# Performance work log

Hardware: AMD Instinct MI355X
Metric: run time of the kernel (lower is better)

Reference implementation:

```python
import jax, jax.numpy as jnp
import numpy as np

N_NODES = 100000
N_EDGES = 1000000
IN_FEATS = 256
OUT_FEATS = 64


def setup_inputs() -> dict:
    key = jax.random.key(0)
    k1, k2, k3, k4 = jax.random.split(key, 4)
    x = jax.random.normal(k1, (N_NODES, IN_FEATS), dtype=jnp.float32)
    src = jax.random.randint(k2, (N_EDGES,), 0, N_NODES, dtype=jnp.int64)
    dst = jax.random.randint(k3, (N_EDGES,), 0, N_NODES, dtype=jnp.int64)
    # Glorot-style init as in dgl GraphConv
    W = jax.random.normal(k4, (IN_FEATS, OUT_FEATS), dtype=jnp.float32) * (2.0 / (IN_FEATS + OUT_FEATS)) ** 0.5
    b = jnp.zeros((OUT_FEATS,), dtype=jnp.float32)
    return {"x": x, "src": src, "dst": dst, "W": W, "b": b}


def reference(x, src, dst, W, b):
    # dgl GraphConv with norm='both':
    #   h = D_in^{-1/2} * A * D_out^{-1/2} * X * W + b
    # in_feats > out_feats -> dense transform first, then sparse aggregation.
    n = x.shape[0]
    e_ones = jnp.ones(src.shape[0], dtype=x.dtype)
    deg_out = jnp.clip(jax.ops.segment_sum(e_ones, src, num_segments=n), 1.0)  # [N]
    deg_in = jnp.clip(jax.ops.segment_sum(e_ones, dst, num_segments=n), 1.0)   # [N]
    h = (x * deg_out[:, None] ** -0.5) @ W                 # [N, out]
    agg = jax.ops.segment_sum(h[src], dst, num_segments=n)  # SpMM: [N, out]
    return agg * deg_in[:, None] ** -0.5 + b
```

## Files before the change

kernel.cpp:

```cpp
#include <hip/hip_runtime.h>

#define IN_F 256
#define OUT_F 64
#define BLK1 1024
#define BKT 128
#define CAP 4096

typedef __attribute__((ext_vector_type(8))) short s16x8;
typedef __attribute__((ext_vector_type(4))) float f32x4;
typedef __attribute__((ext_vector_type(4))) unsigned u32x4;

__device__ __forceinline__ unsigned short bf16_rne(float f) {
    unsigned u = __builtin_bit_cast(unsigned, f);
    u += 0x7FFFu + ((u >> 16) & 1u);
    return (unsigned short)(u >> 16);
}
__device__ __forceinline__ float bf16_lo(unsigned u) {
    return __builtin_bit_cast(float, u << 16);
}
__device__ __forceinline__ float bf16_hi(unsigned u) {
    return __builtin_bit_cast(float, u & 0xFFFF0000u);
}
__device__ __forceinline__ unsigned pk2(float a, float b) {
    unsigned r;
    asm("v_cvt_pk_bf16_f32 %0, %1, %2" : "=v"(r) : "v"(a), "v"(b));
    return r;
}

__global__ __launch_bounds__(512) void k_coarse(const int* __restrict__ src,
                                                const int* __restrict__ dst,
                                                int* __restrict__ cnt,
                                                int nb, int ne) {
    __shared__ int hD[1024], hS[1024];
    const int blk = blockIdx.x, tid = threadIdx.x;
    for (int i = tid; i < 1024; i += 512) { hD[i] = 0; hS[i] = 0; }
    __syncthreads();
    const int epb = (ne + BLK1 - 1) / BLK1;
    const int e0 = blk * epb, e1 = min(ne, e0 + epb);
    for (int e = e0 + tid; e < e1; e += 512) {
        atomicAdd(&hD[dst[e] >> 7], 1);
        atomicAdd(&hS[src[e] >> 7], 1);
    }
    __syncthreads();
    for (int bb = tid; bb < nb; bb += 512) {
        cnt[bb * BLK1 + blk] = hD[bb];
        cnt[(nb + bb) * BLK1 + blk] = hS[bb];
    }
}

__global__ __launch_bounds__(256) void k_scan1(const int* __restrict__ deg,
                                               int* __restrict__ excl,
                                               int* __restrict__ partials) {
    __shared__ int sd[256];
    const int tid = threadIdx.x;
    const int idx = blockIdx.x * 2048 + tid * 8;
    int4 va = *(const int4*)&deg[idx];
    int4 vb = *(const int4*)&deg[idx + 4];
    const int tsum = va.x + va.y + va.z + va.w + vb.x + vb.y + vb.z + vb.w;
    sd[tid] = tsum;
    __syncthreads();
    for (int off = 1; off < 256; off <<= 1) {
        int t = (tid >= off) ? sd[tid - off] : 0;
        __syncthreads();
        sd[tid] += t;
        __syncthreads();
    }
    int run = sd[tid] - tsum;
    if (tid == 255) partials[blockIdx.x] = sd[255];
    int4 oa, ob;
    oa.x = run; run += va.x;
    oa.y = run; run += va.y;
    oa.z = run; run += va.z;
    oa.w = run; run += va.w;
    ob.x = run; run += vb.x;
    ob.y = run; run += vb.y;
    ob.z = run; run += vb.z;
    ob.w = run;
    *(int4*)&excl[idx] = oa;
    *(int4*)&excl[idx + 4] = ob;
}

__global__ __launch_bounds__(1024) void k_scan2(int* __restrict__ partials, int nb) {
    __shared__ int sd[1024];
    const int tid = threadIdx.x;
    const int v = (tid < nb) ? partials[tid] : 0;
    sd[tid] = v;
    __syncthreads();
    for (int off = 1; off < 1024; off <<= 1) {
        int t = (tid >= off) ? sd[tid - off] : 0;
        __syncthreads();
        sd[tid] += t;
        __syncthreads();
    }
    if (tid < nb) partials[tid] = sd[tid] - v;
}

__global__ __launch_bounds__(512) void k_part(const int* __restrict__ src,
                                              const int* __restrict__ dst,
                                              const int* __restrict__ cnt,
                                              const int* __restrict__ partials,
                                              unsigned* __restrict__ tmpD,
                                              unsigned char* __restrict__ tmpS,
                                              int nb, int ne) {
    __shared__ int cD[1024], cS[1024];
    const int blk = blockIdx.x, tid = threadIdx.x;
    for (int bb = tid; bb < nb; bb += 512) {
        int iD = bb * BLK1 + blk;
        int iS = (nb + bb) * BLK1 + blk;
        cD[bb] = cnt[iD] + partials[iD >> 11];
        cS[bb] = cnt[iS] + partials[iS >> 11];
    }
    __syncthreads();
    const int epb = (ne + BLK1 - 1) / BLK1;
    const int e0 = blk * epb, e1 = min(ne, e0 + epb);
    for (int e = e0 + tid; e < e1; e += 512) {
        int d = dst[e], s = src[e];
        int pD = atomicAdd(&cD[d >> 7], 1);
        tmpD[pD] = ((unsigned)(d & 127) << 17) | (unsigned)s;
        int pS = atomicAdd(&cS[s >> 7], 1);
        tmpS[pS - ne] = (unsigned char)(s & 127);
    }
}

__global__ __launch_bounds__(256) void k_fine_src(const int* __restrict__ cnt,
                                                  const int* __restrict__ partials,
                                                  const unsigned char* __restrict__ tmpS,
                                                  int* __restrict__ deg_out,
                                                  int n, int nb, int ne) {
    __shared__ int hist[BKT];
    const int b = blockIdx.x, tid = threadIdx.x;
    const int ib = (nb + b) * BLK1;
    const int base = cnt[ib] + partials[ib >> 11] - ne;
    const int ie = (nb + b + 1) * BLK1;
    const int end = (b + 1 < nb) ? (cnt[ie] + partials[ie >> 11] - ne) : ne;
    if (tid < BKT) hist[tid] = 0;
    __syncthreads();
    for (int i = base + tid; i < end; i += 256)
        atomicAdd(&hist[tmpS[i] & 127u], 1);
    __syncthreads();
    const int node = b * BKT + tid;
    if (tid < BKT && node < n) deg_out[node] = hist[tid];
}

__global__ __launch_bounds__(256, 4) void k_gemm(const float* __restrict__ x,
                                                 const float* __restrict__ W,
                                                 const int* __restrict__ deg_out,
                                                 unsigned short* __restrict__ h, int n) {
    __shared__ char lds[32768];
    const int tid = threadIdx.x;
    const int lane = tid & 63;
    const int wid = tid >> 6;

    {
        const int f = tid & 63;
        const int kg = (tid >> 6) * 64;
        const int swz = (f & 7) << 4;
#pragma unroll
        for (int j = 0; j < 16; ++j) {
            const int k0 = kg + j * 4;
            float w0 = W[(k0 + 0) * OUT_F + f];
            float w1 = W[(k0 + 1) * OUT_F + f];
            float w2 = W[(k0 + 2) * OUT_F + f];
            float w3 = W[(k0 + 3) * OUT_F + f];
            uint2 p;
            p.x = pk2(w0, w1);
            p.y = pk2(w2, w3);
            *(uint2*)(lds + f * 512 + ((k0 * 2) ^ swz)) = p;
        }
    }
    __syncthreads();

    const int r15 = lane & 15;
    const int q = lane >> 4;
    const int bswz = (r15 & 7) << 4;
    const int b_base = r15 * 512;
    const int rq = q * 4;

#pragma unroll
    for (int p = 0; p < 2; ++p) {
        const int row = blockIdx.x * 128 + p * 64 + wid * 16 + r15;
        const int rowc = min(row, n - 1);
        const float* xr = x + (size_t)rowc * IN_F + q * 8;

        f32x4 acc0 = {0.f, 0.f, 0.f, 0.f};
        f32x4 acc1 = acc0, acc2 = acc0, acc3 = acc0;

#pragma unroll
        for (int kk = 0; kk < 8; ++kk) {
            float4 a0 = *(const float4*)(xr + kk * 32);
            float4 a1 = *(const float4*)(xr + kk * 32 + 4);
            u32x4 au;
            au[0] = pk2(a0.x, a0.y);
            au[1] = pk2(a0.z, a0.w);
            au[2] = pk2(a1.x, a1.y);
            au[3] = pk2(a1.z, a1.w);
            s16x8 a = __builtin_bit_cast(s16x8, au);
            const int off = (q * 16 + kk * 64) ^ bswz;
            s16x8 b0 = *(const s16x8*)(lds + b_base + off);
            s16x8 b1 = *(const s16x8*)(lds + b_base + 8192 + off);
            s16x8 b2 = *(const s16x8*)(lds + b_base + 16384 + off);
            s16x8 b3 = *(const s16x8*)(lds + b_base + 24576 + off);
            acc0 = __builtin_amdgcn_mfma_f32_16x16x32_bf16(a, b0, acc0, 0, 0, 0);
            acc1 = __builtin_amdgcn_mfma_f32_16x16x32_bf16(a, b1, acc1, 0, 0, 0);
            acc2 = __builtin_amdgcn_mfma_f32_16x16x32_bf16(a, b2, acc2, 0, 0, 0);
            acc3 = __builtin_amdgcn_mfma_f32_16x16x32_bf16(a, b3, acc3, 0, 0, 0);
        }

#pragma unroll
        for (int j = 0; j < 4; ++j) {
            const int grow = blockIdx.x * 128 + p * 64 + wid * 16 + rq + j;
            if (grow < n) {
                const float s = rsqrtf(fmaxf((float)deg_out[grow], 1.0f));
                unsigned short* hp = h + (size_t)grow * OUT_F + r15;
                hp[0]  = bf16_rne(acc0[j] * s);
                hp[16] = bf16_rne(acc1[j] * s);
                hp[32] = bf16_rne(acc2[j] * s);
                hp[48] = bf16_rne(acc3[j] * s);
            }
        }
    }
}

__global__ __launch_bounds__(512) void k_agg(const int* __restrict__ cnt,
                                             const int* __restrict__ partials,
                                             const unsigned* __restrict__ tmpD,
                                             const unsigned* __restrict__ h32,
                                             const float* __restrict__ b,
                                             float* __restrict__ out,
                                             int n, int nb, int ne) {
    __shared__ int hist[BKT], sd[BKT], cur[BKT], stt[BKT];
    __shared__ unsigned raw[CAP];
    __shared__ int eidx[CAP];
    const int bkt = blockIdx.x, tid = threadIdx.x;
    const int ib = bkt * BLK1;
    const int base = cnt[ib] + partials[ib >> 11];
    const int ie = (bkt + 1) * BLK1;
    const int end = (bkt + 1 < nb) ? (cnt[ie] + partials[ie >> 11]) : ne;
    const int cnt_e = min(end - base, CAP);

    if (tid < BKT) hist[tid] = 0;
    __syncthreads();
    for (int i = tid; i < cnt_e; i += 512) {
        unsigned v = tmpD[base + i];
        raw[i] = v;
        atomicAdd(&hist[v >> 17], 1);
    }
    __syncthreads();
    int dg0 = 0;
    if (tid < BKT) { dg0 = hist[tid]; sd[tid] = dg0; }
    __syncthreads();
    for (int off = 1; off < BKT; off <<= 1) {
        int t = 0;
        if (tid < BKT && tid >= off) t = sd[tid - off];
        __syncthreads();
        if (tid < BKT) sd[tid] += t;
        __syncthreads();
    }
    if (tid < BKT) {
        const int excl = sd[tid] - dg0;
        cur[tid] = excl;
        stt[tid] = excl;
    }
    __syncthreads();
    for (int i = tid; i < cnt_e; i += 512) {
        unsigned v = raw[i];
        int pos = atomicAdd(&cur[v >> 17], 1);
        eidx[min(pos, CAP - 1)] = (int)(v & 0x1FFFFu);
    }
    __syncthreads();

    const int wid = tid >> 6, lane = tid & 63;
    const int f2 = lane & 31, half = lane >> 5;
    for (int nd = wid; nd < BKT; nd += 8) {
        const int node = bkt * BKT + nd;
        if (node >= n) continue;
        const int st = stt[nd];
        const int dg = hist[nd];
        float a0 = 0.f, a1 = 0.f, c0 = 0.f, c1 = 0.f;
        float d0 = 0.f, d1 = 0.f, e0 = 0.f, e1 = 0.f;
        int i = 0;
        const int dg8 = dg & ~7;
        for (; i < dg8; i += 8) {
            int s0 = eidx[st + i + half];
            int s1 = eidx[st + i + 2 + half];
            int s2 = eidx[st + i + 4 + half];
            int s3 = eidx[st + i + 6 + half];
            unsigned u0 = h32[s0 * 32 + f2];
            unsigned u1 = h32[s1 * 32 + f2];
            unsigned u2 = h32[s2 * 32 + f2];
            unsigned u3 = h32[s3 * 32 + f2];
            a0 += bf16_lo(u0); a1 += bf16_hi(u0);
            c0 += bf16_lo(u1); c1 += bf16_hi(u1);
            d0 += bf16_lo(u2); d1 += bf16_hi(u2);
            e0 += bf16_lo(u3); e1 += bf16_hi(u3);
        }
        for (; i < dg; i += 2) {
            const int e = i + half;
            const bool v = e < dg;
            int s = eidx[st + (v ? e : i)];
            unsigned u = h32[s * 32 + f2];
            if (v) { a0 += bf16_lo(u); a1 += bf16_hi(u); }
        }
        a0 += c0; a1 += c1;
        d0 += e0; d1 += e1;
        a0 += d0; a1 += d1;
        a0 += __shfl_xor(a0, 32, 64);
        a1 += __shfl_xor(a1, 32, 64);
        if (half == 0) {
            const float scale = rsqrtf(fmaxf((float)dg, 1.0f));
            float2 v;
            v.x = a0 * scale + b[f2 * 2];
            v.y = a1 * scale + b[f2 * 2 + 1];
            *(float2*)&out[(size_t)node * OUT_F + f2 * 2] = v;
        }
    }
}

extern "C" void kernel_launch(void* const* d_in, const int* in_sizes, int n_in,
                              void* d_out, int out_size, void* d_ws, size_t ws_size,
                              hipStream_t stream) {
    const float* x   = (const float*)d_in[0];
    const int*   src = (const int*)d_in[1];
    const int*   dst = (const int*)d_in[2];
    const float* W   = (const float*)d_in[3];
    const float* b   = (const float*)d_in[4];
    float* out = (float*)d_out;

    const int n  = in_sizes[0] / IN_F;
    const int ne = in_sizes[1];

    const int nb = (n + BKT - 1) / BKT;
    const int m  = 2 * nb * BLK1;

    int* cnt          = (int*)d_ws;
    int* partials     = cnt + m;
    unsigned* tmpD    = (unsigned*)(partials + 1024);
    unsigned char* tmpS = (unsigned char*)(tmpD + ne);
    int* deg_out      = (int*)(tmpS + ((ne + 15) & ~15));
    unsigned short* h = (unsigned short*)(deg_out + n);

    const int nb_scan = m / 2048;

    k_coarse<<<BLK1, 512, 0, stream>>>(src, dst, cnt, nb, ne);
    k_scan1<<<nb_scan, 256, 0, stream>>>(cnt, cnt, partials);
    k_scan2<<<1, 1024, 0, stream>>>(partials, nb_scan);
    k_part<<<BLK1, 512, 0, stream>>>(src, dst, cnt, partials, tmpD, tmpS, nb, ne);
    k_fine_src<<<nb, 256, 0, stream>>>(cnt, partials, tmpS, deg_out, n, nb, ne);
    k_gemm<<<(n + 127) / 128, 256, 0, stream>>>(x, W, deg_out, h, n);
    k_agg<<<nb, 512, 0, stream>>>(cnt, partials, tmpD, (const unsigned*)h, b, out, n, nb, ne);
}
```

Measured before the change: 117.4 us.

## Fuse out-degree histogram into GEMM kernel and halve partition block count

Removes the separate k_fine_src kernel: each GEMM block now builds the out-degree histogram for its 128-node bucket in shared memory and applies the rsqrt scaling from LDS, dropping a launch and the deg_out global round trip. The partitioning pipeline also moves from 1024 blocks of 512 threads to 512 blocks of 256 threads. That shrinks the count matrix and the scan, with the scan indexing adjusted to match. The price is that the histogram pass now sits at the start of the GEMM, and the partition kernels have less parallelism.

```diff
diff --git a/kernel.cpp b/kernel.cpp
--- a/kernel.cpp
+++ b/kernel.cpp
@@ -2,7 +2,7 @@
 
 #define IN_F 256
 #define OUT_F 64
-#define BLK1 1024
+#define BLK1 512
 #define BKT 128
 #define CAP 4096
 
@@ -27,22 +27,22 @@
     return r;
 }
 
-__global__ __launch_bounds__(512) void k_coarse(const int* __restrict__ src,
+__global__ __launch_bounds__(256) void k_coarse(const int* __restrict__ src,
                                                 const int* __restrict__ dst,
                                                 int* __restrict__ cnt,
                                                 int nb, int ne) {
     __shared__ int hD[1024], hS[1024];
     const int blk = blockIdx.x, tid = threadIdx.x;
-    for (int i = tid; i < 1024; i += 512) { hD[i] = 0; hS[i] = 0; }
+    for (int i = tid; i < 1024; i += 256) { hD[i] = 0; hS[i] = 0; }
     __syncthreads();
     const int epb = (ne + BLK1 - 1) / BLK1;
     const int e0 = blk * epb, e1 = min(ne, e0 + epb);
-    for (int e = e0 + tid; e < e1; e += 512) {
+    for (int e = e0 + tid; e < e1; e += 256) {
         atomicAdd(&hD[dst[e] >> 7], 1);
         atomicAdd(&hS[src[e] >> 7], 1);
     }
     __syncthreads();
-    for (int bb = tid; bb < nb; bb += 512) {
+    for (int bb = tid; bb < nb; bb += 256) {
         cnt[bb * BLK1 + blk] = hD[bb];
         cnt[(nb + bb) * BLK1 + blk] = hS[bb];
     }
@@ -53,10 +53,9 @@
                                                int* __restrict__ partials) {
     __shared__ int sd[256];
     const int tid = threadIdx.x;
-    const int idx = blockIdx.x * 2048 + tid * 8;
-    int4 va = *(const int4*)&deg[idx];
-    int4 vb = *(const int4*)&deg[idx + 4];
-    const int tsum = va.x + va.y + va.z + va.w + vb.x + vb.y + vb.z + vb.w;
+    const int idx = blockIdx.x * 1024 + tid * 4;
+    int4 v = *(const int4*)&deg[idx];
+    const int tsum = v.x + v.y + v.z + v.w;
     sd[tid] = tsum;
     __syncthreads();
     for (int off = 1; off < 256; off <<= 1) {
@@ -67,17 +66,12 @@
     }
     int run = sd[tid] - tsum;
     if (tid == 255) partials[blockIdx.x] = sd[255];
-    int4 oa, ob;
-    oa.x = run; run += va.x;
-    oa.y = run; run += va.y;
-    oa.z = run; run += va.z;
-    oa.w = run; run += va.w;
-    ob.x = run; run += vb.x;
-    ob.y = run; run += vb.y;
-    ob.z = run; run += vb.z;
-    ob.w = run;
-    *(int4*)&excl[idx] = oa;
-    *(int4*)&excl[idx + 4] = ob;
+    int4 o;
+    o.x = run; run += v.x;
+    o.y = run; run += v.y;
+    o.z = run; run += v.z;
+    o.w = run;
+    *(int4*)&excl[idx] = o;
 }
 
 __global__ __launch_bounds__(1024) void k_scan2(int* __restrict__ partials, int nb) {
@@ -95,7 +89,7 @@
     if (tid < nb) partials[tid] = sd[tid] - v;
 }
 
-__global__ __launch_bounds__(512) void k_part(const int* __restrict__ src,
+__global__ __launch_bounds__(256) void k_part(const int* __restrict__ src,
                                               const int* __restrict__ dst,
                                               const int* __restrict__ cnt,
                                               const int* __restrict__ partials,
@@ -104,16 +98,16 @@
                                               int nb, int ne) {
     __shared__ int cD[1024], cS[1024];
     const int blk = blockIdx.x, tid = threadIdx.x;
-    for (int bb = tid; bb < nb; bb += 512) {
+    for (int bb = tid; bb < nb; bb += 256) {
         int iD = bb * BLK1 + blk;
         int iS = (nb + bb) * BLK1 + blk;
-        cD[bb] = cnt[iD] + partials[iD >> 11];
-        cS[bb] = cnt[iS] + partials[iS >> 11];
+        cD[bb] = cnt[iD] + partials[iD >> 10];
+        cS[bb] = cnt[iS] + partials[iS >> 10];
     }
     __syncthreads();
     const int epb = (ne + BLK1 - 1) / BLK1;
     const int e0 = blk * epb, e1 = min(ne, e0 + epb);
-    for (int e = e0 + tid; e < e1; e += 512) {
+    for (int e = e0 + tid; e < e1; e += 256) {
         int d = dst[e], s = src[e];
         int pD = atomicAdd(&cD[d >> 7], 1);
         tmpD[pD] = ((unsigned)(d & 127) << 17) | (unsigned)s;
@@ -122,35 +116,30 @@
     }
 }
 
-__global__ __launch_bounds__(256) void k_fine_src(const int* __restrict__ cnt,
-                                                  const int* __restrict__ partials,
-                                                  const unsigned char* __restrict__ tmpS,
-                                                  int* __restrict__ deg_out,
-                                                  int n, int nb, int ne) {
-    __shared__ int hist[BKT];
-    const int b = blockIdx.x, tid = threadIdx.x;
-    const int ib = (nb + b) * BLK1;
-    const int base = cnt[ib] + partials[ib >> 11] - ne;
-    const int ie = (nb + b + 1) * BLK1;
-    const int end = (b + 1 < nb) ? (cnt[ie] + partials[ie >> 11] - ne) : ne;
-    if (tid < BKT) hist[tid] = 0;
-    __syncthreads();
-    for (int i = base + tid; i < end; i += 256)
-        atomicAdd(&hist[tmpS[i] & 127u], 1);
-    __syncthreads();
-    const int node = b * BKT + tid;
-    if (tid < BKT && node < n) deg_out[node] = hist[tid];
-}
-
 __global__ __launch_bounds__(256, 4) void k_gemm(const float* __restrict__ x,
                                                  const float* __restrict__ W,
-                                                 const int* __restrict__ deg_out,
-                                                 unsigned short* __restrict__ h, int n) {
+                                                 const int* __restrict__ cnt,
+                                                 const int* __restrict__ partials,
+                                                 const unsigned char* __restrict__ tmpS,
+                                                 unsigned short* __restrict__ h,
+                                                 int n, int nb, int ne) {
     __shared__ char lds[32768];
+    __shared__ int hist[BKT];
     const int tid = threadIdx.x;
     const int lane = tid & 63;
     const int wid = tid >> 6;
-
+    const int b = blockIdx.x;
+
+    if (tid < BKT) hist[tid] = 0;
+    __syncthreads();
+    {
+        const int ib = (nb + b) * BLK1;
+        const int base = cnt[ib] + partials[ib >> 10] - ne;
+        const int ie2 = (nb + b + 1) * BLK1;
+        const int end = (b + 1 < nb) ? (cnt[ie2] + partials[ie2 >> 10] - ne) : ne;
+        for (int i = base + tid; i < end; i += 256)
+            atomicAdd(&hist[tmpS[i] & 127u], 1);
+    }
     {
         const int f = tid & 63;
         const int kg = (tid >> 6) * 64;
@@ -178,7 +167,7 @@
 
 #pragma unroll
     for (int p = 0; p < 2; ++p) {
-        const int row = blockIdx.x * 128 + p * 64 + wid * 16 + r15;
+        const int row = b * 128 + p * 64 + wid * 16 + r15;
         const int rowc = min(row, n - 1);
         const float* xr = x + (size_t)rowc * IN_F + q * 8;
 
@@ -208,9 +197,9 @@
 
 #pragma unroll
         for (int j = 0; j < 4; ++j) {
-            const int grow = blockIdx.x * 128 + p * 64 + wid * 16 + rq + j;
+            const int grow = b * 128 + p * 64 + wid * 16 + rq + j;
             if (grow < n) {
-                const float s = rsqrtf(fmaxf((float)deg_out[grow], 1.0f));
+                const float s = rsqrtf(fmaxf((float)hist[grow & 127], 1.0f));
                 unsigned short* hp = h + (size_t)grow * OUT_F + r15;
                 hp[0]  = bf16_rne(acc0[j] * s);
                 hp[16] = bf16_rne(acc1[j] * s);
@@ -233,9 +222,9 @@
     __shared__ int eidx[CAP];
     const int bkt = blockIdx.x, tid = threadIdx.x;
     const int ib = bkt * BLK1;
-    const int base = cnt[ib] + partials[ib >> 11];
+    const int base = cnt[ib] + partials[ib >> 10];
     const int ie = (bkt + 1) * BLK1;
-    const int end = (bkt + 1 < nb) ? (cnt[ie] + partials[ie >> 11]) : ne;
+    const int end = (bkt + 1 < nb) ? (cnt[ie] + partials[ie >> 10]) : ne;
     const int cnt_e = min(end - base, CAP);
 
     if (tid < BKT) hist[tid] = 0;
@@ -336,16 +325,14 @@
     int* partials     = cnt + m;
     unsigned* tmpD    = (unsigned*)(partials + 1024);
     unsigned char* tmpS = (unsigned char*)(tmpD + ne);
-    int* deg_out      = (int*)(tmpS + ((ne + 15) & ~15));
-    unsigned short* h = (unsigned short*)(deg_out + n);
-
-    const int nb_scan = m / 2048;
-
-    k_coarse<<<BLK1, 512, 0, stream>>>(src, dst, cnt, nb, ne);
+    unsigned short* h = (unsigned short*)(tmpS + (((size_t)ne + 15) & ~(size_t)15));
+
+    const int nb_scan = m / 1024;
+
+    k_coarse<<<BLK1, 256, 0, stream>>>(src, dst, cnt, nb, ne);
     k_scan1<<<nb_scan, 256, 0, stream>>>(cnt, cnt, partials);
     k_scan2<<<1, 1024, 0, stream>>>(partials, nb_scan);
-    k_part<<<BLK1, 512, 0, stream>>>(src, dst, cnt, partials, tmpD, tmpS, nb, ne);
-    k_fine_src<<<nb, 256, 0, stream>>>(cnt, partials, tmpS, deg_out, n, nb, ne);
-    k_gemm<<<(n + 127) / 128, 256, 0, stream>>>(x, W, deg_out, h, n);
+    k_part<<<BLK1, 256, 0, stream>>>(src, dst, cnt, partials, tmpD, tmpS, nb, ne);
+    k_gemm<<<nb, 256, 0, stream>>>(x, W, cnt, partials, tmpS, h, n, nb, ne);
     k_agg<<<nb, 512, 0, stream>>>(cnt, partials, tmpD, (const unsigned*)h, b, out, n, nb, ne);
 }
```

After: 111.7 us. -4.8%, faster.
